# Optimization experiments

Hardware: AMD Instinct MI355X
Metric: run time of the kernel (lower is better)

## Reference

```python
import jax, jax.numpy as jnp
import numpy as np

MAX_K = 70  # 70*5 = 350 = Linear in-features
EPS = 1e-5


def _bn(x, g, b):
    # BatchNorm1d with track_running_stats=False -> always batch stats, biased var
    m = jnp.mean(x, axis=0)
    v = jnp.mean((x - m) ** 2, axis=0)
    return (x - m) * jax.lax.rsqrt(v + EPS) * g + b


def _stack_bind(feat, ccids, n_comps):
    # Pack up to MAX_K member features per connected component: [n_comps, MAX_K*F]
    N, F = feat.shape
    order = jnp.argsort(ccids)              # stable sort by component id
    sc = ccids[order]
    sf = feat[order]
    pos = jnp.arange(N)
    is_start = jnp.concatenate([jnp.ones((1,), bool), sc[1:] != sc[:-1]])
    seg_start = jax.lax.cummax(jnp.where(is_start, pos, 0))
    rank = pos - seg_start                  # index of item within its component
    valid = rank < MAX_K
    comp_idx = jnp.where(valid, sc, n_comps)  # overflow items dropped
    rank_c = jnp.minimum(rank, MAX_K - 1)
    out = jnp.zeros((n_comps + 1, MAX_K, F), feat.dtype)
    out = out.at[comp_idx, rank_c].set(sf, mode='drop')
    return out[:n_comps].reshape(n_comps, MAX_K * F)


def setup_inputs() -> dict:
    key = jax.random.key(0)
    ks = jax.random.split(key, 8)
    N, C, B, NC = 4_000_000, 200_000, 64, 1000
    std = 0.1
    inp = {
        'item_feat': jax.random.normal(ks[0], (N, 5), jnp.float32),
        'ccids': jax.random.randint(ks[1], (N,), 0, C, jnp.int32),
        'imgid': jax.random.randint(ks[2], (C,), 0, B, jnp.int32),
        'W1': jax.random.normal(ks[3], (350, 32), jnp.float32) * std,
        'b1': jnp.zeros((32,), jnp.float32),
        'g1': jnp.ones((32,), jnp.float32),
        'be1': jnp.zeros((32,), jnp.float32),
        'W2': jax.random.normal(ks[4], (32, 64), jnp.float32) * std,
        'b2': jnp.zeros((64,), jnp.float32),
        'g2': jnp.ones((64,), jnp.float32),
        'be2': jnp.zeros((64,), jnp.float32),
        'W3': jax.random.normal(ks[5], (64, 128), jnp.float32) * std,
        'b3': jnp.zeros((128,), jnp.float32),
        'g3': jnp.ones((128,), jnp.float32),
        'be3': jnp.zeros((128,), jnp.float32),
        'W4': jax.random.normal(ks[6], (128, 256), jnp.float32) * std,
        'b4': jnp.zeros((256,), jnp.float32),
        'g4': jnp.ones((256,), jnp.float32),
        'be4': jnp.zeros((256,), jnp.float32),
        'g5': jnp.ones((256,), jnp.float32),
        'be5': jnp.zeros((256,), jnp.float32),
        'Wfc': jax.random.normal(ks[7], (256, NC), jnp.float32) * (1.0 / np.sqrt(256.0)),
        'bfc': jnp.zeros((NC,), jnp.float32),
        'n_comps': C,
        'batch_size': B,
    }
    return inp


def reference(item_feat, ccids, imgid,
              W1, b1, g1, be1, W2, b2, g2, be2,
              W3, b3, g3, be3, W4, b4, g4, be4,
              g5, be5, Wfc, bfc, n_comps, batch_size):
    x = _stack_bind(item_feat, ccids, n_comps)            # [C, 350]
    x = jax.nn.relu(_bn(x @ W1 + b1, g1, be1))
    x = jax.nn.relu(_bn(x @ W2 + b2, g2, be2))
    x = jax.nn.relu(_bn(x @ W3 + b3, g3, be3))
    x = jax.nn.relu(_bn(x @ W4 + b4, g4, be4))            # [C, 256]
    # avg_pool over components per image
    s = jax.ops.segment_sum(x, imgid, num_segments=batch_size)
    cnt = jax.ops.segment_sum(jnp.ones((x.shape[0],), x.dtype), imgid,
                              num_segments=batch_size)
    cnt = jnp.where(cnt < 1, jnp.ones_like(cnt), cnt)
    x = s / cnt[:, None]                                   # [B, 256]
    x = _bn(x, g5, be5)
    x = jax.nn.relu(x @ Wfc + bfc)                         # [B, n_classes]
    return x
```

## Files before the change

kernel.cpp:

```cpp
#include <hip/hip_runtime.h>
#include <hip/hip_bf16.h>
#include <cstdint>
#include <cstddef>

#define MAX_K 70
#define BN_EPS 1e-5f
#define KPAD 360
#define NPOOL 16
#define ACHUNK 2048
#define BCHUNK 2048
#define CCAP 3584
#define NSBMAX 2048
#define NDCOPY 16
#define DSTRIDE 1408

typedef __attribute__((ext_vector_type(4))) float f32x4;
typedef __attribute__((ext_vector_type(8))) short bf16x8;
typedef __attribute__((ext_vector_type(4))) int i32x4;

__device__ inline float loadv(const float* p, size_t i) { return p[i]; }
__device__ inline float loadv(const __hip_bfloat16* p, size_t i) {
    return __bfloat162float(p[i]);
}
__device__ inline void storev(float* p, size_t i, float v) { p[i] = v; }
__device__ inline void storev(__hip_bfloat16* p, size_t i, float v) {
    p[i] = __float2bfloat16(v);
}
__device__ inline float bf2f(unsigned short u) {
    union { unsigned int i; float f; } x; x.i = ((unsigned int)u) << 16; return x.f;
}
__device__ inline unsigned short f2bfu(float f) {
    __hip_bfloat16 h = __float2bfloat16(f);
    return *reinterpret_cast<unsigned short*>(&h);
}

template <int FO>
__device__ inline void bn_make(const double* __restrict__ ds,
                               const double* __restrict__ dq,
                               const float* __restrict__ g,
                               const float* __restrict__ be, int C,
                               float* aSs, float* cSs, int tid) {
    if (tid < FO) {
        double m = 0.0, v = 0.0;
        #pragma unroll
        for (int k = 0; k < NDCOPY; ++k) {
            m += ds[(size_t)k * DSTRIDE + tid];
            v += dq[(size_t)k * DSTRIDE + tid];
        }
        m /= (double)C;
        v = v / (double)C - m * m;
        float rs = rsqrtf((float)v + BN_EPS);
        float a = g[tid] * rs;
        aSs[tid] = a;
        cSs[tid] = be[tid] - (float)m * a;
    }
}

__global__ __launch_bounds__(256) void hist_kernel(
    const i32x4* __restrict__ cc4, int* __restrict__ sbsize,
    const int* __restrict__ imgid, int* __restrict__ pcnt,
    int n4, int C, int cg, int nsb, int B) {
    __shared__ int h[NSBMAX];
    __shared__ int scnt[64];
    int tid = threadIdx.x;
    int nsbtot = 8 * nsb;
    for (int t = tid; t < nsbtot; t += 256) h[t] = 0;
    if (tid < B) scnt[tid] = 0;
    __syncthreads();
    int per = (n4 + gridDim.x - 1) / gridDim.x;
    int q0 = blockIdx.x * per, q1 = min(q0 + per, n4);
    for (int q = q0 + tid; q < q1; q += 256) {
        i32x4 v = cc4[q];
        #pragma unroll
        for (int e = 0; e < 4; ++e) {
            int c = v[e];
            int g = c / cg;
            int loc = c - g * cg;
            atomicAdd(&h[g * nsb + (loc >> 7)], 1);
        }
    }
    for (int i = blockIdx.x * 256 + tid; i < C; i += gridDim.x * 256)
        atomicAdd(&scnt[imgid[i]], 1);
    __syncthreads();
    for (int t = tid; t < nsbtot; t += 256) {
        int v = h[t];
        if (v) atomicAdd(&sbsize[t], v);
    }
    if (tid < B) {
        int v = scnt[tid];
        if (v) atomicAdd(&pcnt[tid], v);
    }
}

__global__ void prep_kernel(const float* __restrict__ W4,
                            const float* __restrict__ W1,
                            unsigned short* __restrict__ w4t,
                            unsigned short* __restrict__ w1t) {
    int idx = blockIdx.x * 256 + threadIdx.x;
    if (idx < 32768) {
        int n = idx >> 7, k = idx & 127;
        w4t[idx] = f2bfu(W4[k * 256 + n]);
    } else if (idx < 32768 + 32 * 352) {
        int j = idx - 32768;
        int ch = j / 352, k = j - ch * 352;
        w1t[j] = (k < 350) ? f2bfu(W1[k * 32 + ch]) : 0;
    }
}

__global__ __launch_bounds__(256) void scan_sb(
    const int* __restrict__ sbsize, int* __restrict__ sboff,
    int* __restrict__ sbcur, int* __restrict__ bcur,
    int nsbtot, int nsb, int N) {
    __shared__ int sc[256];
    int tid = threadIdx.x;
    int base = tid * 8;
    int v[8];
    int tsum = 0;
    #pragma unroll
    for (int e = 0; e < 8; ++e) {
        int i = base + e;
        v[e] = (i < nsbtot) ? sbsize[i] : 0;
        tsum += v[e];
    }
    sc[tid] = tsum;
    __syncthreads();
    for (int d = 1; d < 256; d <<= 1) {
        int t = (tid >= d) ? sc[tid - d] : 0;
        __syncthreads();
        sc[tid] += t;
        __syncthreads();
    }
    int run = sc[tid] - tsum;
    #pragma unroll
    for (int e = 0; e < 8; ++e) {
        int i = base + e;
        if (i < nsbtot) { sboff[i] = run; sbcur[i] = run; }
        run += v[e];
    }
    if (tid == 0) sboff[nsbtot] = N;
    __syncthreads();
    if (tid < 8) bcur[tid] = (tid * nsb < nsbtot) ? sboff[tid * nsb] : N;
}

__global__ __launch_bounds__(256) void bucketA_kernel(
    const int* __restrict__ ccids, const float* __restrict__ feat,
    int* __restrict__ bcur, i32x4* __restrict__ bstage, int N, int cg) {
    __shared__ int scnt[8], scur[8];
    int tid = threadIdx.x;
    int base = blockIdx.x * ACHUNK;
    if (tid < 8) scnt[tid] = 0;
    __syncthreads();
    int myg[8], myloc[8];
    #pragma unroll
    for (int k = 0; k < 8; ++k) {
        int i = base + k * 256 + tid;
        int g = -1, loc = 0;
        if (i < N) {
            int c = ccids[i];
            g = c / cg;
            loc = c - g * cg;
            atomicAdd(&scnt[g], 1);
        }
        myg[k] = g; myloc[k] = loc;
    }
    __syncthreads();
    if (tid < 8) scur[tid] = atomicAdd(&bcur[tid], scnt[tid]);
    __syncthreads();
    #pragma unroll
    for (int k = 0; k < 8; ++k) {
        int i = base + k * 256 + tid;
        if (i < N) {
            const float* fp = &feat[(size_t)i * 5];
            float f0 = fp[0], f1 = fp[1], f2 = fp[2], f3 = fp[3], f4 = fp[4];
            int slot = atomicAdd(&scur[myg[k]], 1);
            i32x4 r;
            r[0] = i;
            r[1] = (int)(((unsigned)f2bfu(f0)) | (((unsigned)f2bfu(f1)) << 16));
            r[2] = (int)(((unsigned)f2bfu(f2)) | (((unsigned)f2bfu(f3)) << 16));
            r[3] = (int)(((unsigned)f2bfu(f4)) | (((unsigned)myloc[k]) << 16));
            bstage[slot] = r;
        }
    }
}

__global__ __launch_bounds__(256) void bucketB2_kernel(
    const i32x4* __restrict__ bstage, const int* __restrict__ sboff,
    int* __restrict__ sbcur, i32x4* __restrict__ bstage2,
    int N, int C, int cg, int nsb) {
    __shared__ int scntA[256];
    __shared__ int spref[256];
    __shared__ int scur[256];
    __shared__ int sgbase[256];
    __shared__ unsigned char sbof[BCHUNK];
    __shared__ i32x4 stage2[BCHUNK];
    int tid = threadIdx.x;
    int g  = blockIdx.x & 7;
    int k  = blockIdx.x >> 3;
    int nk = gridDim.x >> 3;
    int bs = sboff[g * nsb];
    int be = sboff[(g + 1) * nsb];
    for (int cbase = bs + k * BCHUNK; cbase < be; cbase += nk * BCHUNK) {
        int cnt_ = min(BCHUNK, be - cbase);
        scntA[tid] = 0;
        __syncthreads();
        i32x4 it[8]; int sb[8];
        #pragma unroll
        for (int u = 0; u < 8; ++u) {
            int t = u * 256 + tid;
            sb[u] = -1;
            if (t < cnt_) {
                it[u] = bstage[cbase + t];
                int loc = (int)(((unsigned)it[u][3]) >> 16);
                sb[u] = loc >> 7;
                atomicAdd(&scntA[sb[u]], 1);
            }
        }
        __syncthreads();
        spref[tid] = scntA[tid];
        __syncthreads();
        for (int d = 1; d < 256; d <<= 1) {
            int t = (tid >= d) ? spref[tid - d] : 0;
            __syncthreads();
            spref[tid] += t;
            __syncthreads();
        }
        int excl = spref[tid] - scntA[tid];
        __syncthreads();
        spref[tid] = excl;
        scur[tid] = 0;
        if (tid < nsb && scntA[tid] > 0)
            sgbase[tid] = atomicAdd(&sbcur[g * nsb + tid], scntA[tid]);
        __syncthreads();
        #pragma unroll
        for (int u = 0; u < 8; ++u) {
            if (sb[u] >= 0) {
                int w = atomicAdd(&scur[sb[u]], 1);
                int pos = spref[sb[u]] + w;
                stage2[pos] = it[u];
                sbof[pos] = (unsigned char)sb[u];
            }
        }
        __syncthreads();
        for (int t = tid; t < cnt_; t += 256) {
            int s = sbof[t];
            bstage2[sgbase[s] + (t - spref[s])] = stage2[t];
        }
        __syncthreads();
    }
}

__global__ __launch_bounds__(256) void bucketC_kernel(
    const i32x4* __restrict__ bstage2, const int* __restrict__ sboff,
    i32x4* __restrict__ srec, int* __restrict__ cnt, int* __restrict__ off,
    int N, int C, int cg, int nsb) {
    int g  = blockIdx.x >> 8;
    int sb = blockIdx.x & 255;
    if (sb >= nsb) return;
    int c0 = g * cg + sb * 128;
    if (c0 >= C) return;
    int gend = min(g * cg + cg, C);
    int c1 = min(c0 + 128, gend);
    int nc = c1 - c0;
    int gsb = g * nsb + sb;
    int p0 = sboff[gsb];
    int p1 = sboff[gsb + 1];
    int count = p1 - p0;
    int tid = threadIdx.x;
    __shared__ i32x4 stg[CCAP];
    __shared__ int ccnt[128], cpref[128], ccur[128];
    if (count <= CCAP) {
        if (tid < 128) ccnt[tid] = 0;
        __syncthreads();
        for (int t = tid; t < count; t += 256) {
            int loc = (int)(((unsigned)bstage2[p0 + t][3]) >> 16);
            atomicAdd(&ccnt[loc - sb * 128], 1);
        }
        __syncthreads();
        if (tid < 128) cpref[tid] = ccnt[tid];
        __syncthreads();
        for (int d = 1; d < 128; d <<= 1) {
            int t = (tid >= d && tid < 128) ? cpref[tid - d] : 0;
            __syncthreads();
            if (tid < 128) cpref[tid] += t;
            __syncthreads();
        }
        if (tid < 128) { cpref[tid] -= ccnt[tid]; ccur[tid] = 0; }
        __syncthreads();
        if (tid < nc) {
            cnt[c0 + tid] = ccnt[tid];
            off[c0 + tid] = p0 + cpref[tid];
        }
        for (int t = tid; t < count; t += 256) {
            i32x4 r = bstage2[p0 + t];
            int cl = (int)(((unsigned)r[3]) >> 16) - sb * 128;
            int w = atomicAdd(&ccur[cl], 1);
            stg[cpref[cl] + w] = r;
        }
        __syncthreads();
        for (int t = tid; t < count; t += 256) {
            i32x4 r = stg[t];
            int cl = (int)(((unsigned)r[3]) >> 16) - sb * 128;
            int b0 = cpref[cl], cn = ccnt[cl];
            int my = r[0];
            int rk = 0;
            for (int j = 0; j < cn; ++j)
                rk += (stg[b0 + j][0] < my) ? 1 : 0;
            srec[p0 + b0 + rk] = r;
        }
    } else {
        for (int cl = tid; cl < nc; cl += 256) {
            int myloc = sb * 128 + cl;
            int cc = 0, bb = 0;
            for (int j = 0; j < count; ++j) {
                int ol = (int)(((unsigned)bstage2[p0 + j][3]) >> 16);
                cc += (ol == myloc) ? 1 : 0;
                bb += (ol < myloc) ? 1 : 0;
            }
            cnt[c0 + cl] = cc;
            off[c0 + cl] = p0 + bb;
        }
        for (int t = tid; t < count; t += 256) {
            i32x4 r = bstage2[p0 + t];
            int myloc = (int)(((unsigned)r[3]) >> 16);
            int my = r[0];
            int rk = 0, base = 0;
            for (int j = 0; j < count; ++j) {
                i32x4 o = bstage2[p0 + j];
                int ol = (int)(((unsigned)o[3]) >> 16);
                if (ol == myloc) rk += (o[0] < my) ? 1 : 0;
                else if (ol < myloc) base += 1;
            }
            srec[p0 + base + rk] = r;
        }
    }
}

__global__ __launch_bounds__(256) void layer1_mfma(
    const i32x4* __restrict__ srec, const int* __restrict__ cnt,
    const int* __restrict__ off,
    const unsigned short* __restrict__ w1t, const float* __restrict__ b1,
    float* __restrict__ z1, double* __restrict__ dsum,
    double* __restrict__ dsq, int C) {
    __shared__ unsigned short xtile[4][16][KPAD];
    __shared__ float sps[4][32], spq[4][32];
    int tid  = threadIdx.x;
    int w    = tid >> 6;
    int lane = tid & 63;
    int cbase = blockIdx.x * 64 + w * 16;

    unsigned int* xz = (unsigned int*)&xtile[w][0][0];
    for (int t = lane; t < 16 * (KPAD / 2); t += 64) xz[t] = 0u;

    int myc = 0, myo = 0;
    {
        int comp = cbase + (lane & 15);
        if (comp < C) { myc = cnt[comp]; myo = off[comp]; }
    }
    int fl[16], bs[16];
    #pragma unroll
    for (int s = 0; s < 16; ++s) {
        fl[s] = __shfl(myc, s);
        bs[s] = __shfl(myo, s);
    }
    __syncthreads();
    #pragma unroll
    for (int s = 0; s < 16; ++s) {
        int lim = min(fl[s], MAX_K);
        for (int e = lane; e < lim; e += 64) {
            i32x4 r = srec[bs[s] + e];
            unsigned short* xp = &xtile[w][s][e * 5];
            unsigned int y1 = (unsigned int)r[1];
            unsigned int y2 = (unsigned int)r[2];
            unsigned int y3 = (unsigned int)r[3];
            xp[0] = (unsigned short)(y1 & 0xffff);
            xp[1] = (unsigned short)(y1 >> 16);
            xp[2] = (unsigned short)(y2 & 0xffff);
            xp[3] = (unsigned short)(y2 >> 16);
            xp[4] = (unsigned short)(y3 & 0xffff);
        }
    }
    __syncthreads();

    int l15 = lane & 15, l4 = lane >> 4;
    f32x4 acc0 = {0.f, 0.f, 0.f, 0.f};
    f32x4 acc1 = {0.f, 0.f, 0.f, 0.f};
    const unsigned short* xbase = &xtile[w][l15][0];
    #pragma unroll
    for (int ks = 0; ks < 11; ++ks) {
        int k0 = ks * 32 + l4 * 8;
        bf16x8 a  = *(const bf16x8*)&xbase[k0];
        bf16x8 b0 = *(const bf16x8*)&w1t[(size_t)l15 * 352 + k0];
        bf16x8 bv = *(const bf16x8*)&w1t[(size_t)(16 + l15) * 352 + k0];
        acc0 = __builtin_amdgcn_mfma_f32_16x16x32_bf16(a, b0, acc0, 0, 0, 0);
        acc1 = __builtin_amdgcn_mfma_f32_16x16x32_bf16(a, bv, acc1, 0, 0, 0);
    }
    float bias0 = b1[l15];
    float bias1 = b1[16 + l15];
    float s0 = 0.f, q0 = 0.f, s1 = 0.f, q1 = 0.f;
    #pragma unroll
    for (int r = 0; r < 4; ++r) {
        int comp = cbase + l4 * 4 + r;
        if (comp < C) {
            float z0 = acc0[r] + bias0;
            float z1v = acc1[r] + bias1;
            z1[(size_t)comp * 32 + l15]      = z0;
            z1[(size_t)comp * 32 + 16 + l15] = z1v;
            s0 += z0; q0 += z0 * z0;
            s1 += z1v; q1 += z1v * z1v;
        }
    }
    s0 += __shfl_xor(s0, 16); s0 += __shfl_xor(s0, 32);
    q0 += __shfl_xor(q0, 16); q0 += __shfl_xor(q0, 32);
    s1 += __shfl_xor(s1, 16); s1 += __shfl_xor(s1, 32);
    q1 += __shfl_xor(q1, 16); q1 += __shfl_xor(q1, 32);
    if (lane < 16) {
        sps[w][l15] = s0;      spq[w][l15] = q0;
        sps[w][16 + l15] = s1; spq[w][16 + l15] = q1;
    }
    __syncthreads();
    if (tid < 32) {
        float s = sps[0][tid] + sps[1][tid] + sps[2][tid] + sps[3][tid];
        float q = spq[0][tid] + spq[1][tid] + spq[2][tid] + spq[3][tid];
        size_t cb = (size_t)(blockIdx.x & (NDCOPY - 1)) * DSTRIDE;
        unsafeAtomicAdd(&dsum[cb + tid], (double)s);
        unsafeAtomicAdd(&dsq[cb + tid],  (double)q);
    }
}

template <typename TI, typename TO, int FI, int FO, int CT, int RT>
__global__ __launch_bounds__(256) void layer_kernel(
    const TI* __restrict__ zin, const float* __restrict__ W,
    const float* __restrict__ bias,
    const double* __restrict__ dsI, const double* __restrict__ dqI,
    const float* __restrict__ g, const float* __restrict__ be,
    TO* __restrict__ zout,
    double* __restrict__ dsO, double* __restrict__ dqO, int C) {
    constexpr int CHG  = FO / CT;
    constexpr int NSUB = 256 / CHG;
    constexpr int R    = NSUB * RT;
    __shared__ float h[R][FI + 1];
    __shared__ float sps[NSUB * FO];
    __shared__ float spq[NSUB * FO];
    __shared__ float aSs[FI], cSs[FI];
    int tid = threadIdx.x;
    int c0 = blockIdx.x * R;
    bn_make<FI>(dsI, dqI, g, be, C, aSs, cSs, tid);
    __syncthreads();
    for (int t = tid; t < R * FI; t += 256) {
        int r = t / FI, k = t % FI;
        int c = c0 + r;
        float v = (c < C) ? loadv(zin, (size_t)c * FI + k) : 0.f;
        h[r][k] = fmaxf(fmaf(aSs[k], v, cSs[k]), 0.f);
    }
    __syncthreads();
    int cg  = tid % CHG;
    int sub = tid / CHG;
    int chbase = cg * CT;
    float acc[RT][CT];
    #pragma unroll
    for (int i = 0; i < RT; ++i)
        #pragma unroll
        for (int j = 0; j < CT; ++j) acc[i][j] = 0.f;
    for (int k = 0; k < FI; ++k) {
        float wv[CT];
        #pragma unroll
        for (int j4 = 0; j4 < CT; j4 += 4) {
            const float4 wq = *reinterpret_cast<const float4*>(
                &W[(size_t)k * FO + chbase + j4]);
            wv[j4 + 0] = wq.x; wv[j4 + 1] = wq.y;
            wv[j4 + 2] = wq.z; wv[j4 + 3] = wq.w;
        }
        #pragma unroll
        for (int i = 0; i < RT; ++i) {
            float hv = h[sub * RT + i][k];
            #pragma unroll
            for (int j = 0; j < CT; ++j) acc[i][j] = fmaf(hv, wv[j], acc[i][j]);
        }
    }
    float ps[CT], pq[CT];
    #pragma unroll
    for (int j = 0; j < CT; ++j) { ps[j] = 0.f; pq[j] = 0.f; }
    #pragma unroll
    for (int i = 0; i < RT; ++i) {
        int c = c0 + sub * RT + i;
        if (c < C) {
            #pragma unroll
            for (int j = 0; j < CT; ++j) {
                float z = acc[i][j] + bias[chbase + j];
                storev(zout, (size_t)c * FO + chbase + j, z);
                ps[j] += z;
                pq[j] += z * z;
            }
        }
    }
    #pragma unroll
    for (int j = 0; j < CT; ++j) {
        sps[sub * FO + chbase + j] = ps[j];
        spq[sub * FO + chbase + j] = pq[j];
    }
    __syncthreads();
    if (tid < FO) {
        float s = 0.f, q = 0.f;
        #pragma unroll
        for (int s2 = 0; s2 < NSUB; ++s2) {
            s += sps[s2 * FO + tid];
            q += spq[s2 * FO + tid];
        }
        size_t cb = (size_t)(blockIdx.x & (NDCOPY - 1)) * DSTRIDE;
        unsafeAtomicAdd(&dsO[cb + tid], (double)s);
        unsafeAtomicAdd(&dqO[cb + tid], (double)q);
    }
}

__global__ __launch_bounds__(256) void layer4_mfma(
    const __hip_bfloat16* __restrict__ z3, const unsigned short* __restrict__ w4t,
    const float* __restrict__ b4,
    const double* __restrict__ dsI, const double* __restrict__ dqI,
    const float* __restrict__ g, const float* __restrict__ be,
    __hip_bfloat16* __restrict__ z4,
    double* __restrict__ dsum, double* __restrict__ dsq, int C) {
    __shared__ float sps[2][256];
    __shared__ float spq[2][256];
    __shared__ float aSs[128], cSs[128];
    int tid = threadIdx.x, wid = tid >> 6, lane = tid & 63;
    int wm = wid >> 1, wn = wid & 1;
    int c0 = blockIdx.x * 64;
    int l15 = lane & 15, l4 = lane >> 4;
    const unsigned short* z3u = (const unsigned short*)z3;
    bn_make<128>(dsI, dqI, g, be, C, aSs, cSs, tid);
    __syncthreads();

    f32x4 acc[2][8];
    #pragma unroll
    for (int mi = 0; mi < 2; ++mi)
        #pragma unroll
        for (int ni = 0; ni < 8; ++ni) acc[mi][ni] = (f32x4){0.f, 0.f, 0.f, 0.f};

    int rowA0 = c0 + wm * 32 + l15;
    #pragma unroll
    for (int ks = 0; ks < 4; ++ks) {
        int k0 = ks * 32 + l4 * 8;
        float sc[8], cc[8];
        #pragma unroll
        for (int j = 0; j < 8; ++j) { sc[j] = aSs[k0 + j]; cc[j] = cSs[k0 + j]; }
        bf16x8 afrag[2];
        #pragma unroll
        for (int mi = 0; mi < 2; ++mi) {
            int r = rowA0 + mi * 16;
            int rc = (r < C) ? r : (C - 1);
            bf16x8 raw = *(const bf16x8*)&z3u[(size_t)rc * 128 + k0];
            bf16x8 af;
            #pragma unroll
            for (int j = 0; j < 8; ++j) {
                float v = bf2f((unsigned short)raw[j]);
                float hx = fmaxf(fmaf(sc[j], v, cc[j]), 0.f);
                af[j] = (short)f2bfu((r < C) ? hx : 0.f);
            }
            afrag[mi] = af;
        }
        bf16x8 bfrag[8];
        #pragma unroll
        for (int ni = 0; ni < 8; ++ni) {
            int n = wn * 128 + ni * 16 + l15;
            bfrag[ni] = *(const bf16x8*)&w4t[(size_t)n * 128 + k0];
        }
        #pragma unroll
        for (int mi = 0; mi < 2; ++mi)
            #pragma unroll
            for (int ni = 0; ni < 8; ++ni)
                acc[mi][ni] = __builtin_amdgcn_mfma_f32_16x16x32_bf16(
                    afrag[mi], bfrag[ni], acc[mi][ni], 0, 0, 0);
    }
    unsigned short* z4u = (unsigned short*)z4;
    #pragma unroll
    for (int ni = 0; ni < 8; ++ni) {
        int col = wn * 128 + ni * 16 + l15;
        float bv = b4[col];
        float s = 0.f, q = 0.f;
        #pragma unroll
        for (int mi = 0; mi < 2; ++mi) {
            #pragma unroll
            for (int r = 0; r < 4; ++r) {
                int row = c0 + wm * 32 + mi * 16 + l4 * 4 + r;
                float z = acc[mi][ni][r] + bv;
                if (row < C) {
                    z4u[(size_t)row * 256 + col] = f2bfu(z);
                    s += z;
                    q += z * z;
                }
            }
        }
        s += __shfl_xor(s, 16); s += __shfl_xor(s, 32);
        q += __shfl_xor(q, 16); q += __shfl_xor(q, 32);
        if (lane < 16) { sps[wm][col] = s; spq[wm][col] = q; }
    }
    __syncthreads();
    if (tid < 256) {
        float s = sps[0][tid] + sps[1][tid];
        float q = spq[0][tid] + spq[1][tid];
        size_t cb = (size_t)(blockIdx.x & (NDCOPY - 1)) * DSTRIDE;
        unsafeAtomicAdd(&dsum[cb + tid], (double)s);
        unsafeAtomicAdd(&dsq[cb + tid],  (double)q);
    }
}

__global__ __launch_bounds__(256) void pool_kernel(
    const __hip_bfloat16* __restrict__ z4, const int* __restrict__ imgid,
    const double* __restrict__ dsI, const double* __restrict__ dqI,
    const float* __restrict__ g, const float* __restrict__ be,
    float* __restrict__ pool, int C, int B) {
    __shared__ float spool[64 * 256];
    __shared__ float aSs[256], cSs[256];
    int tid = threadIdx.x;
    int nb = B * 256;
    bn_make<256>(dsI, dqI, g, be, C, aSs, cSs, tid);
    for (int t = tid; t < nb; t += 256) spool[t] = 0.f;
    __syncthreads();
    float a = aSs[tid], cc = cSs[tid];
    int per  = (C + gridDim.x - 1) / gridDim.x;
    int cbeg = blockIdx.x * per;
    int cend = min(cbeg + per, C);
    int c = cbeg;
    for (; c + 16 <= cend; c += 16) {
        float v[16];
        int im[16];
        #pragma unroll
        for (int u = 0; u < 16; ++u) {
            im[u] = imgid[c + u];
            v[u] = loadv(z4, (size_t)(c + u) * 256 + tid);
        }
        #pragma unroll
        for (int u = 0; u < 16; ++u) {
            float hv = fmaxf(fmaf(a, v[u], cc), 0.f);
            spool[im[u] * 256 + tid] += hv;
        }
    }
    for (; c < cend; ++c) {
        int img = imgid[c];
        float v = loadv(z4, (size_t)c * 256 + tid);
        float hv = fmaxf(fmaf(a, v, cc), 0.f);
        spool[img * 256 + tid] += hv;
    }
    __syncthreads();
    float* dst = pool + (size_t)(blockIdx.x & (NPOOL - 1)) * nb;
    int start = ((int)blockIdx.x * 2048) % nb;
    for (int t0 = 0; t0 < nb; t0 += 256) {
        int t = (start + t0 + tid) % nb;
        unsafeAtomicAdd(&dst[t], spool[t]);
    }
}

__global__ void bn5_kernel(const float* __restrict__ pool,
                           const int* __restrict__ pcnt,
                           const float* __restrict__ g5,
                           const float* __restrict__ be5,
                           float* __restrict__ y, int B) {
    int ch = threadIdx.x;
    int nb = B * 256;
    double s = 0.0, s2 = 0.0;
    float vals[64];
    for (int b = 0; b < B; ++b) {
        float v = 0.f;
        #pragma unroll
        for (int k = 0; k < NPOOL; ++k) v += pool[k * nb + b * 256 + ch];
        float c = (float)pcnt[b]; if (c < 1.f) c = 1.f;
        v /= c;
        vals[b] = v;
        s += (double)v; s2 += (double)v * (double)v;
    }
    double m = s / (double)B;
    double var = s2 / (double)B - m * m;
    float rs = rsqrtf((float)var + BN_EPS);
    float a = g5[ch] * rs;
    float cc = be5[ch] - (float)m * a;
    for (int b = 0; b < B; ++b)
        y[b * 256 + ch] = fmaf(a, vals[b], cc);
}

__global__ __launch_bounds__(256) void fc_kernel(
    const float* __restrict__ y, const float* __restrict__ Wfc,
    const float* __restrict__ bfc, float* __restrict__ out, int NC) {
    int b = blockIdx.y;
    int ch = blockIdx.x * 256 + threadIdx.x;
    __shared__ float sy[256];
    sy[threadIdx.x] = y[b * 256 + threadIdx.x];
    __syncthreads();
    if (ch < NC) {
        float acc = bfc[ch];
        for (int k = 0; k < 256; ++k)
            acc = fmaf(sy[k], Wfc[(size_t)k * NC + ch], acc);
        out[(size_t)b * NC + ch] = fmaxf(acc, 0.f);
    }
}

extern "C" void kernel_launch(void* const* d_in, const int* in_sizes, int n_in,
                              void* d_out, int out_size, void* d_ws,
                              size_t ws_size, hipStream_t stream) {
    const float* item_feat = (const float*)d_in[0];
    const int*   ccids     = (const int*)d_in[1];
    const int*   imgid     = (const int*)d_in[2];
    const float* W1  = (const float*)d_in[3];
    const float* b1  = (const float*)d_in[4];
    const float* g1  = (const float*)d_in[5];
    const float* be1 = (const float*)d_in[6];
    const float* W2  = (const float*)d_in[7];
    const float* b2  = (const float*)d_in[8];
    const float* g2  = (const float*)d_in[9];
    const float* be2 = (const float*)d_in[10];
    const float* W3  = (const float*)d_in[11];
    const float* b3  = (const float*)d_in[12];
    const float* g3  = (const float*)d_in[13];
    const float* be3 = (const float*)d_in[14];
    const float* W4  = (const float*)d_in[15];
    const float* b4  = (const float*)d_in[16];
    const float* g4  = (const float*)d_in[17];
    const float* be4 = (const float*)d_in[18];
    const float* g5  = (const float*)d_in[19];
    const float* be5 = (const float*)d_in[20];
    const float* Wfc = (const float*)d_in[21];
    const float* bfc = (const float*)d_in[22];
    float* out = (float*)d_out;

    const int N  = in_sizes[1];
    const int C  = in_sizes[2];
    const int NC = in_sizes[22];
    const int B  = out_size / NC;

    uint8_t* ws = (uint8_t*)d_ws;
    size_t off_ = 0;
    auto alloc = [&](size_t bytes) -> void* {
        void* p = (void*)(ws + off_);
        off_ += (bytes + 255) & ~(size_t)255;
        return p;
    };
    int*    sbsize = (int*)alloc((size_t)NSBMAX * 4);
    double* dstats = (double*)alloc((size_t)NDCOPY * DSTRIDE * 8);
    int*    pcnt   = (int*)alloc((size_t)B * 4);
    float*  pool   = (float*)alloc((size_t)NPOOL * B * 256 * 4);
    size_t zeroBytes = off_;
    float*  y      = (float*)alloc((size_t)B * 256 * 4);
    int*    cnt    = (int*)alloc((size_t)C * 4);
    int*    off    = (int*)alloc((size_t)C * 4);
    int*    sboff  = (int*)alloc((size_t)(NSBMAX + 1) * 4);
    int*    sbcur  = (int*)alloc((size_t)NSBMAX * 4);
    int*    bcur   = (int*)alloc((size_t)8 * 4);
    unsigned short* w4t = (unsigned short*)alloc((size_t)256 * 128 * 2);
    unsigned short* w1t = (unsigned short*)alloc((size_t)32 * 352 * 2);
    void* regionA = alloc((size_t)N * 16);
    void* regionB = alloc((size_t)C * 256 * 2);
    (void)ws_size;

    i32x4*           bstage  = (i32x4*)regionB;
    i32x4*           bstage2 = (i32x4*)regionA;
    i32x4*           srec    = (i32x4*)regionB;
    float*           z1      = (float*)regionA;
    __hip_bfloat16*  z3      = (__hip_bfloat16*)regionA;
    __hip_bfloat16*  z2      = (__hip_bfloat16*)regionB;
    __hip_bfloat16*  z4      = (__hip_bfloat16*)regionB;

    double *ds1 = dstats +   0, *dq1 = dstats +  32;
    double *ds2 = dstats +  64, *dq2 = dstats + 128;
    double *ds3 = dstats + 192, *dq3 = dstats + 320;
    double *ds4 = dstats + 448, *dq4 = dstats + 704;

    const int cg     = (C + 7) / 8;
    const int nsb    = (cg + 127) / 128;
    const int nsbtot = 8 * nsb;

    hipMemsetAsync(ws, 0, zeroBytes, stream);
    hist_kernel<<<512, 256, 0, stream>>>((const i32x4*)ccids, sbsize,
                                         imgid, pcnt, N / 4, C, cg, nsb, B);
    prep_kernel<<<172, 256, 0, stream>>>(W4, W1, w4t, w1t);
    scan_sb<<<1, 256, 0, stream>>>(sbsize, sboff, sbcur, bcur, nsbtot, nsb, N);
    bucketA_kernel<<<(N + ACHUNK - 1) / ACHUNK, 256, 0, stream>>>(
        ccids, item_feat, bcur, bstage, N, cg);
    bucketB2_kernel<<<1960, 256, 0, stream>>>(bstage, sboff, sbcur, bstage2,
                                              N, C, cg, nsb);
    bucketC_kernel<<<8 * 256, 256, 0, stream>>>(bstage2, sboff, srec,
                                                cnt, off, N, C, cg, nsb);

    layer1_mfma<<<(C + 63) / 64, 256, 0, stream>>>(srec, cnt, off,
                                                   w1t, b1, z1, ds1, dq1, C);

    layer_kernel<float, __hip_bfloat16, 32, 64, 4, 8>
        <<<(C + 127) / 128, 256, 0, stream>>>(z1, W2, b2, ds1, dq1, g1, be1,
                                              z2, ds2, dq2, C);
    layer_kernel<__hip_bfloat16, __hip_bfloat16, 64, 128, 4, 8>
        <<<(C + 63) / 64, 256, 0, stream>>>(z2, W3, b3, ds2, dq2, g2, be2,
                                            z3, ds3, dq3, C);
    layer4_mfma<<<(C + 63) / 64, 256, 0, stream>>>(z3, w4t, b4, ds3, dq3,
                                                   g3, be3, z4, ds4, dq4, C);

    pool_kernel<<<512, 256, 0, stream>>>(z4, imgid, ds4, dq4, g4, be4,
                                         pool, C, B);
    bn5_kernel<<<1, 256, 0, stream>>>(pool, pcnt, g5, be5, y, B);

    dim3 fcg((NC + 255) / 256, B);
    fc_kernel<<<fcg, 256, 0, stream>>>(y, Wfc, bfc, out, NC);
}
```

Measured before the change: 618.6 us.

## Use float BN-stat atomics and separate finalize kernels for BN scales

Switches the batch-norm sum and sum-of-squares accumulators from double to float atomics and spreads them over 64 copies instead of 16 to reduce contention. Per-block computation of the BN scale and shift is moved out of every consumer block into tiny single-block finalize kernels that write the scale and shift once. This removes redundant double-precision reductions in every block but adds four extra launches. Float accumulation of sum of squares over 200k rows risks precision loss in the variance.

```diff
diff --git a/kernel.cpp b/kernel.cpp
--- a/kernel.cpp
+++ b/kernel.cpp
@@ -11,7 +11,7 @@
 #define BCHUNK 2048
 #define CCAP 3584
 #define NSBMAX 2048
-#define NDCOPY 16
+#define NDCOPY 64
 #define DSTRIDE 1408
 
 typedef __attribute__((ext_vector_type(4))) float f32x4;
@@ -32,28 +32,6 @@
 __device__ inline unsigned short f2bfu(float f) {
     __hip_bfloat16 h = __float2bfloat16(f);
     return *reinterpret_cast<unsigned short*>(&h);
-}
-
-template <int FO>
-__device__ inline void bn_make(const double* __restrict__ ds,
-                               const double* __restrict__ dq,
-                               const float* __restrict__ g,
-                               const float* __restrict__ be, int C,
-                               float* aSs, float* cSs, int tid) {
-    if (tid < FO) {
-        double m = 0.0, v = 0.0;
-        #pragma unroll
-        for (int k = 0; k < NDCOPY; ++k) {
-            m += ds[(size_t)k * DSTRIDE + tid];
-            v += dq[(size_t)k * DSTRIDE + tid];
-        }
-        m /= (double)C;
-        v = v / (double)C - m * m;
-        float rs = rsqrtf((float)v + BN_EPS);
-        float a = g[tid] * rs;
-        aSs[tid] = a;
-        cSs[tid] = be[tid] - (float)m * a;
-    }
 }
 
 __global__ __launch_bounds__(256) void hist_kernel(
@@ -104,6 +82,30 @@
         int j = idx - 32768;
         int ch = j / 352, k = j - ch * 352;
         w1t[j] = (k < 350) ? f2bfu(W1[k * 32 + ch]) : 0;
+    }
+}
+
+template <int FO>
+__global__ void finalize_kernel(const float* __restrict__ ds,
+                                const float* __restrict__ dq,
+                                const float* __restrict__ g,
+                                const float* __restrict__ be,
+                                float* __restrict__ aS, float* __restrict__ cS,
+                                int C) {
+    int ch = threadIdx.x;
+    if (ch < FO) {
+        float s = 0.f, q = 0.f;
+        #pragma unroll
+        for (int k = 0; k < NDCOPY; ++k) {
+            s += ds[(size_t)k * DSTRIDE + ch];
+            q += dq[(size_t)k * DSTRIDE + ch];
+        }
+        double m = (double)s / (double)C;
+        double v = (double)q / (double)C - m * m;
+        float rs = rsqrtf((float)v + BN_EPS);
+        float a = g[ch] * rs;
+        aS[ch] = a;
+        cS[ch] = be[ch] - (float)m * a;
     }
 }
 
@@ -339,8 +341,8 @@
     const i32x4* __restrict__ srec, const int* __restrict__ cnt,
     const int* __restrict__ off,
     const unsigned short* __restrict__ w1t, const float* __restrict__ b1,
-    float* __restrict__ z1, double* __restrict__ dsum,
-    double* __restrict__ dsq, int C) {
+    float* __restrict__ z1, float* __restrict__ dsum,
+    float* __restrict__ dsq, int C) {
     __shared__ unsigned short xtile[4][16][KPAD];
     __shared__ float sps[4][32], spq[4][32];
     int tid  = threadIdx.x;
@@ -422,8 +424,8 @@
         float s = sps[0][tid] + sps[1][tid] + sps[2][tid] + sps[3][tid];
         float q = spq[0][tid] + spq[1][tid] + spq[2][tid] + spq[3][tid];
         size_t cb = (size_t)(blockIdx.x & (NDCOPY - 1)) * DSTRIDE;
-        unsafeAtomicAdd(&dsum[cb + tid], (double)s);
-        unsafeAtomicAdd(&dsq[cb + tid],  (double)q);
+        unsafeAtomicAdd(&dsum[cb + tid], s);
+        unsafeAtomicAdd(&dsq[cb + tid],  q);
     }
 }
 
@@ -431,10 +433,9 @@
 __global__ __launch_bounds__(256) void layer_kernel(
     const TI* __restrict__ zin, const float* __restrict__ W,
     const float* __restrict__ bias,
-    const double* __restrict__ dsI, const double* __restrict__ dqI,
-    const float* __restrict__ g, const float* __restrict__ be,
+    const float* __restrict__ aS, const float* __restrict__ cS,
     TO* __restrict__ zout,
-    double* __restrict__ dsO, double* __restrict__ dqO, int C) {
+    float* __restrict__ dsO, float* __restrict__ dqO, int C) {
     constexpr int CHG  = FO / CT;
     constexpr int NSUB = 256 / CHG;
     constexpr int R    = NSUB * RT;
@@ -444,7 +445,7 @@
     __shared__ float aSs[FI], cSs[FI];
     int tid = threadIdx.x;
     int c0 = blockIdx.x * R;
-    bn_make<FI>(dsI, dqI, g, be, C, aSs, cSs, tid);
+    if (tid < FI) { aSs[tid] = aS[tid]; cSs[tid] = cS[tid]; }
     __syncthreads();
     for (int t = tid; t < R * FI; t += 256) {
         int r = t / FI, k = t % FI;
@@ -507,18 +508,17 @@
             q += spq[s2 * FO + tid];
         }
         size_t cb = (size_t)(blockIdx.x & (NDCOPY - 1)) * DSTRIDE;
-        unsafeAtomicAdd(&dsO[cb + tid], (double)s);
-        unsafeAtomicAdd(&dqO[cb + tid], (double)q);
+        unsafeAtomicAdd(&dsO[cb + tid], s);
+        unsafeAtomicAdd(&dqO[cb + tid], q);
     }
 }
 
 __global__ __launch_bounds__(256) void layer4_mfma(
     const __hip_bfloat16* __restrict__ z3, const unsigned short* __restrict__ w4t,
     const float* __restrict__ b4,
-    const double* __restrict__ dsI, const double* __restrict__ dqI,
-    const float* __restrict__ g, const float* __restrict__ be,
+    const float* __restrict__ aS, const float* __restrict__ cS,
     __hip_bfloat16* __restrict__ z4,
-    double* __restrict__ dsum, double* __restrict__ dsq, int C) {
+    float* __restrict__ dsum, float* __restrict__ dsq, int C) {
     __shared__ float sps[2][256];
     __shared__ float spq[2][256];
     __shared__ float aSs[128], cSs[128];
@@ -527,7 +527,7 @@
     int c0 = blockIdx.x * 64;
     int l15 = lane & 15, l4 = lane >> 4;
     const unsigned short* z3u = (const unsigned short*)z3;
-    bn_make<128>(dsI, dqI, g, be, C, aSs, cSs, tid);
+    if (tid < 128) { aSs[tid] = aS[tid]; cSs[tid] = cS[tid]; }
     __syncthreads();
 
     f32x4 acc[2][8];
@@ -599,24 +599,21 @@
         float s = sps[0][tid] + sps[1][tid];
         float q = spq[0][tid] + spq[1][tid];
         size_t cb = (size_t)(blockIdx.x & (NDCOPY - 1)) * DSTRIDE;
-        unsafeAtomicAdd(&dsum[cb + tid], (double)s);
-        unsafeAtomicAdd(&dsq[cb + tid],  (double)q);
+        unsafeAtomicAdd(&dsum[cb + tid], s);
+        unsafeAtomicAdd(&dsq[cb + tid],  q);
     }
 }
 
 __global__ __launch_bounds__(256) void pool_kernel(
     const __hip_bfloat16* __restrict__ z4, const int* __restrict__ imgid,
-    const double* __restrict__ dsI, const double* __restrict__ dqI,
-    const float* __restrict__ g, const float* __restrict__ be,
+    const float* __restrict__ aS, const float* __restrict__ cS,
     float* __restrict__ pool, int C, int B) {
     __shared__ float spool[64 * 256];
-    __shared__ float aSs[256], cSs[256];
     int tid = threadIdx.x;
     int nb = B * 256;
-    bn_make<256>(dsI, dqI, g, be, C, aSs, cSs, tid);
     for (int t = tid; t < nb; t += 256) spool[t] = 0.f;
     __syncthreads();
-    float a = aSs[tid], cc = cSs[tid];
+    float a = aS[tid], cc = cS[tid];
     int per  = (C + gridDim.x - 1) / gridDim.x;
     int cbeg = blockIdx.x * per;
     int cend = min(cbeg + per, C);
@@ -734,11 +731,12 @@
         return p;
     };
     int*    sbsize = (int*)alloc((size_t)NSBMAX * 4);
-    double* dstats = (double*)alloc((size_t)NDCOPY * DSTRIDE * 8);
+    float*  fstats = (float*)alloc((size_t)NDCOPY * DSTRIDE * 4);
     int*    pcnt   = (int*)alloc((size_t)B * 4);
     float*  pool   = (float*)alloc((size_t)NPOOL * B * 256 * 4);
     size_t zeroBytes = off_;
     float*  y      = (float*)alloc((size_t)B * 256 * 4);
+    float*  scales = (float*)alloc((size_t)(32 + 64 + 128 + 256) * 2 * 4);
     int*    cnt    = (int*)alloc((size_t)C * 4);
     int*    off    = (int*)alloc((size_t)C * 4);
     int*    sboff  = (int*)alloc((size_t)(NSBMAX + 1) * 4);
@@ -758,10 +756,14 @@
     __hip_bfloat16*  z2      = (__hip_bfloat16*)regionB;
     __hip_bfloat16*  z4      = (__hip_bfloat16*)regionB;
 
-    double *ds1 = dstats +   0, *dq1 = dstats +  32;
-    double *ds2 = dstats +  64, *dq2 = dstats + 128;
-    double *ds3 = dstats + 192, *dq3 = dstats + 320;
-    double *ds4 = dstats + 448, *dq4 = dstats + 704;
+    float *ds1 = fstats +   0, *dq1 = fstats +  32;
+    float *ds2 = fstats +  64, *dq2 = fstats + 128;
+    float *ds3 = fstats + 192, *dq3 = fstats + 320;
+    float *ds4 = fstats + 448, *dq4 = fstats + 704;
+    float *aS1 = scales +   0, *cS1 = scales +  32;
+    float *aS2 = scales +  64, *cS2 = scales + 128;
+    float *aS3 = scales + 192, *cS3 = scales + 320;
+    float *aS4 = scales + 448, *cS4 = scales + 704;
 
     const int cg     = (C + 7) / 8;
     const int nsb    = (cg + 127) / 128;
@@ -781,18 +783,23 @@
 
     layer1_mfma<<<(C + 63) / 64, 256, 0, stream>>>(srec, cnt, off,
                                                    w1t, b1, z1, ds1, dq1, C);
+    finalize_kernel<32><<<1, 32, 0, stream>>>(ds1, dq1, g1, be1, aS1, cS1, C);
 
     layer_kernel<float, __hip_bfloat16, 32, 64, 4, 8>
-        <<<(C + 127) / 128, 256, 0, stream>>>(z1, W2, b2, ds1, dq1, g1, be1,
+        <<<(C + 127) / 128, 256, 0, stream>>>(z1, W2, b2, aS1, cS1,
                                               z2, ds2, dq2, C);
+    finalize_kernel<64><<<1, 64, 0, stream>>>(ds2, dq2, g2, be2, aS2, cS2, C);
+
     layer_kernel<__hip_bfloat16, __hip_bfloat16, 64, 128, 4, 8>
-        <<<(C + 63) / 64, 256, 0, stream>>>(z2, W3, b3, ds2, dq2, g2, be2,
+        <<<(C + 63) / 64, 256, 0, stream>>>(z2, W3, b3, aS2, cS2,
                                             z3, ds3, dq3, C);
-    layer4_mfma<<<(C + 63) / 64, 256, 0, stream>>>(z3, w4t, b4, ds3, dq3,
-                                                   g3, be3, z4, ds4, dq4, C);
-
-    pool_kernel<<<512, 256, 0, stream>>>(z4, imgid, ds4, dq4, g4, be4,
-                                         pool, C, B);
+    finalize_kernel<128><<<1, 128, 0, stream>>>(ds3, dq3, g3, be3, aS3, cS3, C);
+
+    layer4_mfma<<<(C + 63) / 64, 256, 0, stream>>>(z3, w4t, b4, aS3, cS3,
+                                                   z4, ds4, dq4, C);
+    finalize_kernel<256><<<1, 256, 0, stream>>>(ds4, dq4, g4, be4, aS4, cS4, C);
+
+    pool_kernel<<<512, 256, 0, stream>>>(z4, imgid, aS4, cS4, pool, C, B);
     bn5_kernel<<<1, 256, 0, stream>>>(pool, pcnt, g5, be5, y, B);
 
     dim3 fcg((NC + 255) / 256, B);
```

Result: no change. 609.7 us (-1.4%).
